# Optimization experiments

Hardware: AMD Instinct MI355X
Metric: run time of the kernel (lower is better)

Reference implementation:

```python
import jax, jax.numpy as jnp
import numpy as np
import math

B, S, D, H = 2, 2048, 1024, 16
DK = D // H


def setup_inputs() -> dict:
    key = jax.random.key(0)
    k1, k2, k3, k4, k5, k6 = jax.random.split(key, 6)
    scale = 1.0 / math.sqrt(D)
    return {
        "query": jax.random.normal(k1, (B, S, D), dtype=jnp.float32),
        "key": jax.random.normal(k2, (B, S, D), dtype=jnp.float32),
        "value": jax.random.normal(k3, (B, S, D), dtype=jnp.float32),
        "Wqkv": jax.random.normal(k4, (D, D), dtype=jnp.float32) * scale,
        "Wout": jax.random.normal(k5, (D, D), dtype=jnp.float32) * scale,
        "mask": jax.random.randint(k6, (B, 1, S, S), 0, 2, dtype=jnp.int32),
    }


def reference(query, key, value, Wqkv, Wout, mask):
    # Single shared QKV projection (same weight applied to q, k, v), no bias.
    q = query @ Wqkv.T
    k = key @ Wqkv.T
    v = value @ Wqkv.T
    # Faithful to the original: reshape (B, S, D) -> (B, H, S, DK) directly
    # (torch .reshape(n_batches, h, -1, d_k), NOT view+transpose).
    q = q.reshape(B, H, S, DK)
    k = k.reshape(B, H, S, DK)
    v = v.reshape(B, H, S, DK)
    scores = jnp.einsum("bhqd,bhkd->bhqk", q, k) / math.sqrt(DK)
    scores = jnp.where(mask == 0, jnp.float32(-1e9), scores)
    p_attn = jax.nn.softmax(scores, axis=-1)  # dropout is identity in eval
    x = jnp.einsum("bhqk,bhkd->bhqd", p_attn, v)  # [B,H,S,DK]
    x = x.transpose(0, 2, 1, 3).reshape(B, S, H * DK)
    return x @ Wout.T
```

## Files before the change

### kernel.cpp

```cpp
#include <hip/hip_runtime.h>
#include <stdint.h>


typedef __bf16 bf16;
typedef __bf16 bf16x8 __attribute__((ext_vector_type(8)));
typedef __bf16 bf16x4 __attribute__((ext_vector_type(4)));
typedef float f32x4 __attribute__((ext_vector_type(4)));

#define MFMA16(a, b, c) __builtin_amdgcn_mfma_f32_16x16x32_bf16((a), (b), (c), 0, 0, 0)
#define EXP2(x) __builtin_amdgcn_exp2f(x)

static constexpr int BATCH = 2;
static constexpr int SEQ = 2048;
static constexpr int DIM = 1024;
static constexpr int DK = 64;
static constexpr float QSCALE = 0.125f * 1.44269504088896340736f;

__device__ inline void gload16(const void* g, void* l) {
  __builtin_amdgcn_global_load_lds((const __attribute__((address_space(1))) void*)g,
                                   (__attribute__((address_space(3))) void*)l, 16, 0, 0);
}

__global__ __launch_bounds__(256) void mask_bits_kernel(const int* __restrict__ mask,
                                                        unsigned long long* __restrict__ bits) {
  int idx = blockIdx.x * 256 + threadIdx.x;
  int m = mask[idx];
  unsigned long long bal = __ballot(m != 0);
  if ((threadIdx.x & 63) == 0) bits[idx >> 6] = bal;
}

__global__ __launch_bounds__(256) void cvt_bf16_kernel(const float* __restrict__ s0,
                                                       const float* __restrict__ s1,
                                                       const float* __restrict__ s2,
                                                       const float* __restrict__ s3,
                                                       const float* __restrict__ s4,
                                                       bf16* __restrict__ d0, bf16* __restrict__ d1,
                                                       bf16* __restrict__ d2, bf16* __restrict__ d3,
                                                       bf16* __restrict__ d4) {
  const int y = blockIdx.y;
  const float* s = (y == 0) ? s0 : (y == 1) ? s1 : (y == 2) ? s2 : (y == 3) ? s3 : s4;
  bf16* d = (y == 0) ? d0 : (y == 1) ? d1 : (y == 2) ? d2 : (y == 3) ? d3 : d4;
  const int n8 = (y < 3) ? (BATCH * SEQ * DIM / 8) : (DIM * DIM / 8);
  for (int i = blockIdx.x * 256 + threadIdx.x; i < n8; i += gridDim.x * 256) {
    const float4 a = ((const float4*)s)[2 * i];
    const float4 b = ((const float4*)s)[2 * i + 1];
    bf16x8 v;
    v[0] = (bf16)a.x;
    v[1] = (bf16)a.y;
    v[2] = (bf16)a.z;
    v[3] = (bf16)a.w;
    v[4] = (bf16)b.x;
    v[5] = (bf16)b.y;
    v[6] = (bf16)b.z;
    v[7] = (bf16)b.w;
    ((bf16x8*)d)[i] = v;
  }
}

template <int BM, int NBY, int NBZ, typename TC>
__global__ __launch_bounds__(256) void gemm_bt_lds(const bf16* __restrict__ A0,
                                                   const bf16* __restrict__ A1,
                                                   const bf16* __restrict__ A2,
                                                   const bf16* __restrict__ W,
                                                   TC* __restrict__ C0,
                                                   TC* __restrict__ C1,
                                                   TC* __restrict__ C2,
                                                   float scale0) {
  constexpr int K = 1024, N = 1024;
  constexpr int MT = BM / 32;
  constexpr int NB = 8 * NBY * NBZ;
  __shared__ __align__(16) bf16 As[BM * 32];
  __shared__ __align__(16) bf16 Bs[128 * 32];

  const int lin = blockIdx.x + 8 * (blockIdx.y + NBY * blockIdx.z);
  const int l = (lin & 7) * (NB / 8) + (lin >> 3);
  const int lx = l & 7;
  const int lyz = l >> 3;
  const int ly = lyz % NBY;
  const int lz = lyz / NBY;

  const bf16* A = (lz == 0) ? A0 : (lz == 1) ? A1 : A2;
  TC* C = (lz == 0) ? C0 : (lz == 1) ? C1 : C2;
  const float sc = (lz == 0) ? scale0 : 1.0f;

  const int tid = threadIdx.x;
  const int lane = tid & 63;
  const int wv = tid >> 6;
  const int wm = wv >> 1, wn = wv & 1;
  const int lrow = lane & 15, quad = lane >> 4;
  const int m0 = ly * BM, n0 = lx * 128;

  const int r0 = tid >> 2, c0 = (tid & 3) * 8;
  const bf16* pa0 = A + (size_t)(m0 + r0) * K + c0;
  const bf16* pb0 = W + (size_t)(n0 + r0) * K + c0;
  const bf16* pb1 = W + (size_t)(n0 + 64 + r0) * K + c0;
  bf16* la0 = &As[tid * 8];
  bf16* lb0 = &Bs[tid * 8];
  bf16* lb1 = &Bs[2048 + tid * 8];
  const bf16* pa1 = nullptr;
  bf16* la1 = nullptr;
  if constexpr (BM == 128) {
    pa1 = A + (size_t)(m0 + 64 + r0) * K + c0;
    la1 = &As[2048 + tid * 8];
  }

  const f32x4 fz = {0.f, 0.f, 0.f, 0.f};
  f32x4 acc[MT][4];
#pragma unroll
  for (int i = 0; i < MT; ++i)
#pragma unroll
    for (int j = 0; j < 4; ++j) acc[i][j] = fz;

  for (int k0 = 0; k0 < K; k0 += 32) {
    __syncthreads();
    gload16(pa0 + k0, la0);
    if constexpr (BM == 128) gload16(pa1 + k0, la1);
    gload16(pb0 + k0, lb0);
    gload16(pb1 + k0, lb1);
    __syncthreads();
    bf16x8 af[MT], bfr[4];
#pragma unroll
    for (int mt = 0; mt < MT; ++mt)
      af[mt] = *(const bf16x8*)(&As[(wm * (BM / 2) + mt * 16 + lrow) * 32 + quad * 8]);
#pragma unroll
    for (int nt = 0; nt < 4; ++nt)
      bfr[nt] = *(const bf16x8*)(&Bs[(wn * 64 + nt * 16 + lrow) * 32 + quad * 8]);
#pragma unroll
    for (int mt = 0; mt < MT; ++mt)
#pragma unroll
      for (int nt = 0; nt < 4; ++nt) acc[mt][nt] = MFMA16(af[mt], bfr[nt], acc[mt][nt]);
  }

#pragma unroll
  for (int mt = 0; mt < MT; ++mt) {
    const int gm = m0 + wm * (BM / 2) + mt * 16 + quad * 4;
#pragma unroll
    for (int nt = 0; nt < 4; ++nt) {
      const int gn = n0 + wn * 64 + nt * 16 + lrow;
#pragma unroll
      for (int r = 0; r < 4; ++r) C[(size_t)(gm + r) * N + gn] = (TC)(acc[mt][nt][r] * sc);
    }
  }
}

__global__ __launch_bounds__(256, 2) void attn_kernel(const bf16* __restrict__ Qg,
                                                      const bf16* __restrict__ Kg,
                                                      const bf16* __restrict__ Vg,
                                                      const unsigned* __restrict__ bits,
                                                      bf16* __restrict__ Y) {
  constexpr int LQ = 72;
  __shared__ bf16 Qs[128 * LQ];
  __shared__ bf16 Ks[64 * LQ];
  __shared__ bf16 Vts[64 * LQ];
  __shared__ bf16 Ps[4][32 * LQ];

  const int tid = threadIdx.x;
  const int lane = tid & 63;
  const int wv = tid >> 6;
  const int lrow = lane & 15, quad = lane >> 4;
  const int bh = blockIdx.y;
  const int b = bh >> 4, h = bh & 15;
  const int q0 = blockIdx.x * 128;

  const bf16* Qh = Qg + (size_t)bh * (SEQ * DK);
  const bf16* Kh = Kg + (size_t)bh * (SEQ * DK);
  const bf16* Vh = Vg + (size_t)bh * (SEQ * DK);

#pragma unroll
  for (int i = 0; i < 4; ++i) {
    int s = tid + i * 256;
    int row = s >> 3, c8 = (s & 7) * 8;
    *(uint4*)(&Qs[row * LQ + c8]) = *(const uint4*)(Qh + (size_t)(q0 + row) * DK + c8);
  }

  const int krow = tid >> 3;
  const int kc8 = (tid & 7) * 8;
  const bf16* pk0 = Kh + (size_t)krow * DK + kc8;
  const bf16* pk1 = Kh + (size_t)(krow + 32) * DK + kc8;
  const int vn2 = tid & 31;
  const int vk2b = tid >> 5;
  const bf16* pv0 = Vh + (size_t)(vk2b + 0) * 2 * DK + vn2 * 2;
  const bf16* pv1 = Vh + (size_t)(vk2b + 8) * 2 * DK + vn2 * 2;
  const bf16* pv2 = Vh + (size_t)(vk2b + 16) * 2 * DK + vn2 * 2;
  const bf16* pv3 = Vh + (size_t)(vk2b + 24) * 2 * DK + vn2 * 2;

  uint4 kr0, kr1;
  uint32_t va[4], vb[4];

  kr0 = *(const uint4*)(pk0);
  kr1 = *(const uint4*)(pk1);
  va[0] = *(const uint32_t*)(pv0);
  vb[0] = *(const uint32_t*)(pv0 + DK);
  va[1] = *(const uint32_t*)(pv1);
  vb[1] = *(const uint32_t*)(pv1 + DK);
  va[2] = *(const uint32_t*)(pv2);
  vb[2] = *(const uint32_t*)(pv2 + DK);
  va[3] = *(const uint32_t*)(pv3);
  vb[3] = *(const uint32_t*)(pv3 + DK);
  *(uint4*)(&Ks[krow * LQ + kc8]) = kr0;
  *(uint4*)(&Ks[(krow + 32) * LQ + kc8]) = kr1;
#pragma unroll
  for (int i = 0; i < 4; ++i) {
    uint32_t t0 = (va[i] & 0xffffu) | (vb[i] << 16);
    uint32_t t1 = (va[i] >> 16) | (vb[i] & 0xffff0000u);
    *(uint32_t*)(&Vts[(vn2 * 2) * LQ + (vk2b + i * 8) * 2]) = t0;
    *(uint32_t*)(&Vts[(vn2 * 2 + 1) * LQ + (vk2b + i * 8) * 2]) = t1;
  }
  __syncthreads();

  bf16x8 qf[2][2];
#pragma unroll
  for (int nt = 0; nt < 2; ++nt)
#pragma unroll
    for (int ks = 0; ks < 2; ++ks)
      qf[nt][ks] = *(const bf16x8*)(&Qs[(wv * 32 + nt * 16 + lrow) * LQ + ks * 32 + quad * 8]);
  __syncthreads();

  const f32x4 fz = {0.f, 0.f, 0.f, 0.f};
  f32x4 of_t[4][2];
#pragma unroll
  for (int i = 0; i < 4; ++i)
#pragma unroll
    for (int j = 0; j < 2; ++j) of_t[i][j] = fz;
  float lsum[2] = {0.f, 0.f};

  const unsigned* bitrow = bits + (size_t)b * SEQ * (SEQ / 32);

  for (int kt = 0; kt < 32; ++kt) {
    const int cur = kt & 1;
    bf16* kb = cur ? Qs : Ks;
    bf16* vbuf = cur ? (Qs + 64 * LQ) : Vts;
    if (kt + 1 < 32) {
      const size_t adv = (size_t)(kt + 1) * 64 * DK;
      kr0 = *(const uint4*)(pk0 + adv);
      kr1 = *(const uint4*)(pk1 + adv);
      va[0] = *(const uint32_t*)(pv0 + adv);
      vb[0] = *(const uint32_t*)(pv0 + adv + DK);
      va[1] = *(const uint32_t*)(pv1 + adv);
      vb[1] = *(const uint32_t*)(pv1 + adv + DK);
      va[2] = *(const uint32_t*)(pv2 + adv);
      vb[2] = *(const uint32_t*)(pv2 + adv + DK);
      va[3] = *(const uint32_t*)(pv3 + adv);
      vb[3] = *(const uint32_t*)(pv3 + adv + DK);
    }
    uint2 mwn[2];
#pragma unroll
    for (int nt = 0; nt < 2; ++nt) {
      int row = q0 + wv * 32 + nt * 16 + lrow;
      mwn[nt] = *(const uint2*)(bitrow + (size_t)row * (SEQ / 32) + kt * 2);
    }

    f32x4 st[4][2];
#pragma unroll
    for (int mt = 0; mt < 4; ++mt)
#pragma unroll
      for (int nt = 0; nt < 2; ++nt) st[mt][nt] = fz;
#pragma unroll
    for (int ks = 0; ks < 2; ++ks) {
#pragma unroll
      for (int mt = 0; mt < 4; ++mt) {
        bf16x8 kfv = *(const bf16x8*)(kb + (mt * 16 + lrow) * LQ + ks * 32 + quad * 8);
#pragma unroll
        for (int nt = 0; nt < 2; ++nt) st[mt][nt] = MFMA16(kfv, qf[nt][ks], st[mt][nt]);
      }
    }

#pragma unroll
    for (int nt = 0; nt < 2; ++nt) {
      uint32_t ux = mwn[nt].x >> (quad * 4);
      uint32_t uy = mwn[nt].y >> (quad * 4);
      float psum = 0.f;
#pragma unroll
      for (int mt = 0; mt < 4; ++mt) {
        uint32_t u = (mt & 2) ? uy : ux;
        int sh = (mt & 1) << 4;
        bf16x4 pk;
#pragma unroll
        for (int r = 0; r < 4; ++r) {
          float p = EXP2(st[mt][nt][r]);
          p = ((u >> (sh + r)) & 1u) ? p : 0.f;
          psum += p;
          pk[r] = (bf16)p;
        }
        *(bf16x4*)(&Ps[wv][(nt * 16 + lrow) * LQ + mt * 16 + quad * 4]) = pk;
      }
      lsum[nt] += psum;
    }

#pragma unroll
    for (int ks = 0; ks < 2; ++ks) {
      bf16x8 avf[4], bpf[2];
#pragma unroll
      for (int dkt = 0; dkt < 4; ++dkt)
        avf[dkt] = *(const bf16x8*)(vbuf + (dkt * 16 + lrow) * LQ + ks * 32 + quad * 8);
#pragma unroll
      for (int rt = 0; rt < 2; ++rt)
        bpf[rt] = *(const bf16x8*)(&Ps[wv][(rt * 16 + lrow) * LQ + ks * 32 + quad * 8]);
#pragma unroll
      for (int dkt = 0; dkt < 4; ++dkt)
#pragma unroll
        for (int rt = 0; rt < 2; ++rt) of_t[dkt][rt] = MFMA16(avf[dkt], bpf[rt], of_t[dkt][rt]);
    }

    if (kt + 1 < 32) {
      bf16* kbn = cur ? Ks : Qs;
      bf16* vbn = cur ? Vts : (Qs + 64 * LQ);
      *(uint4*)(kbn + krow * LQ + kc8) = kr0;
      *(uint4*)(kbn + (krow + 32) * LQ + kc8) = kr1;
#pragma unroll
      for (int i = 0; i < 4; ++i) {
        uint32_t t0 = (va[i] & 0xffffu) | (vb[i] << 16);
        uint32_t t1 = (va[i] >> 16) | (vb[i] & 0xffff0000u);
        *(uint32_t*)(vbn + (vn2 * 2) * LQ + (vk2b + i * 8) * 2) = t0;
        *(uint32_t*)(vbn + (vn2 * 2 + 1) * LQ + (vk2b + i * 8) * 2) = t1;
      }
    }
    __syncthreads();
  }

  float linv[2];
#pragma unroll
  for (int nt = 0; nt < 2; ++nt) {
    float v = lsum[nt];
    v += __shfl_xor(v, 16);
    v += __shfl_xor(v, 32);
    linv[nt] = 1.0f / fmaxf(v, 1e-20f);
  }

#pragma unroll
  for (int dkt = 0; dkt < 4; ++dkt)
#pragma unroll
    for (int rt = 0; rt < 2; ++rt) {
      bf16x4 o;
#pragma unroll
      for (int j = 0; j < 4; ++j) o[j] = (bf16)(of_t[dkt][rt][j] * linv[rt]);
      const int row = q0 + wv * 32 + rt * 16 + lrow;
      *(bf16x4*)(&Y[((size_t)b * SEQ + row) * DIM + h * 64 + dkt * 16 + quad * 4]) = o;
    }
}

extern "C" void kernel_launch(void* const* d_in, const int* in_sizes, int n_in,
                              void* d_out, int out_size, void* d_ws, size_t ws_size,
                              hipStream_t stream) {
  const float* query = (const float*)d_in[0];
  const float* key = (const float*)d_in[1];
  const float* value = (const float*)d_in[2];
  const float* Wqkv = (const float*)d_in[3];
  const float* Wout = (const float*)d_in[4];
  const int* mask = (const int*)d_in[5];
  float* out = (float*)d_out;

  char* ws = (char*)d_ws;
  bf16* qin = (bf16*)(ws);
  bf16* kin = (bf16*)(ws + 8388608);
  bf16* vin = (bf16*)(ws + 16777216);
  bf16* Wq = (bf16*)(ws + 25165824);
  bf16* Wo = (bf16*)(ws + 27262976);
  bf16* q = (bf16*)(ws + 29360128);
  bf16* k = (bf16*)(ws + 37748736);
  bf16* v = (bf16*)(ws + 46137344);
  bf16* y = (bf16*)(ws);
  unsigned long long* bits64 = (unsigned long long*)(ws + 54525952);

  mask_bits_kernel<<<(BATCH * SEQ * SEQ) / 256, 256, 0, stream>>>(mask, bits64);

  cvt_bf16_kernel<<<dim3(256, 5), 256, 0, stream>>>(query, key, value, Wqkv, Wout,
                                                    qin, kin, vin, Wq, Wo);

  gemm_bt_lds<128, 32, 3, bf16>
      <<<dim3(8, 32, 3), 256, 0, stream>>>(qin, kin, vin, Wq, q, k, v, QSCALE);

  attn_kernel<<<dim3(16, 32), 256, 0, stream>>>(q, k, v, (const unsigned*)bits64, y);

  gemm_bt_lds<64, 64, 1, float>
      <<<dim3(8, 64, 1), 256, 0, stream>>>(y, y, y, Wo, out, out, out, 1.0f);
}
```

Before: 251.3 us.

## Double-buffer GEMM LDS tiles, prefetch mask bits, re-pad V transpose buffers

The projection GEMM now double-buffers its A and W LDS tiles. The next k-slice is issued via global_load_lds before the current slice's MFMAs run, and launch_bounds gains a min-blocks hint. In attention, the mask bit words are loaded one key tile ahead. V-transpose staging moves into two dedicated buffers with a 66-element row stride instead of reusing part of Qs. This aims to hide global latency and reduce LDS bank conflicts, but raises LDS use. The 132-byte row stride also leaves the 16-byte V fragment reads misaligned, which may split or slow those LDS loads.

```diff
diff --git a/kernel.cpp b/kernel.cpp
--- a/kernel.cpp
+++ b/kernel.cpp
@@ -58,19 +58,15 @@
 }
 
 template <int BM, int NBY, int NBZ, typename TC>
-__global__ __launch_bounds__(256) void gemm_bt_lds(const bf16* __restrict__ A0,
-                                                   const bf16* __restrict__ A1,
-                                                   const bf16* __restrict__ A2,
-                                                   const bf16* __restrict__ W,
-                                                   TC* __restrict__ C0,
-                                                   TC* __restrict__ C1,
-                                                   TC* __restrict__ C2,
-                                                   float scale0) {
+__global__ __launch_bounds__(256, (BM == 128) ? 3 : 2) void gemm_bt_lds(
+    const bf16* __restrict__ A0, const bf16* __restrict__ A1, const bf16* __restrict__ A2,
+    const bf16* __restrict__ W, TC* __restrict__ C0, TC* __restrict__ C1, TC* __restrict__ C2,
+    float scale0) {
   constexpr int K = 1024, N = 1024;
   constexpr int MT = BM / 32;
   constexpr int NB = 8 * NBY * NBZ;
-  __shared__ __align__(16) bf16 As[BM * 32];
-  __shared__ __align__(16) bf16 Bs[128 * 32];
+  __shared__ __align__(16) bf16 As[2][BM * 32];
+  __shared__ __align__(16) bf16 Bs[2][128 * 32];
 
   const int lin = blockIdx.x + 8 * (blockIdx.y + NBY * blockIdx.z);
   const int l = (lin & 7) * (NB / 8) + (lin >> 3);
@@ -94,15 +90,8 @@
   const bf16* pa0 = A + (size_t)(m0 + r0) * K + c0;
   const bf16* pb0 = W + (size_t)(n0 + r0) * K + c0;
   const bf16* pb1 = W + (size_t)(n0 + 64 + r0) * K + c0;
-  bf16* la0 = &As[tid * 8];
-  bf16* lb0 = &Bs[tid * 8];
-  bf16* lb1 = &Bs[2048 + tid * 8];
   const bf16* pa1 = nullptr;
-  bf16* la1 = nullptr;
-  if constexpr (BM == 128) {
-    pa1 = A + (size_t)(m0 + 64 + r0) * K + c0;
-    la1 = &As[2048 + tid * 8];
-  }
+  if constexpr (BM == 128) pa1 = A + (size_t)(m0 + 64 + r0) * K + c0;
 
   const f32x4 fz = {0.f, 0.f, 0.f, 0.f};
   f32x4 acc[MT][4];
@@ -111,24 +100,33 @@
 #pragma unroll
     for (int j = 0; j < 4; ++j) acc[i][j] = fz;
 
-  for (int k0 = 0; k0 < K; k0 += 32) {
+  gload16(pa0, &As[0][tid * 8]);
+  if constexpr (BM == 128) gload16(pa1, &As[0][2048 + tid * 8]);
+  gload16(pb0, &Bs[0][tid * 8]);
+  gload16(pb1, &Bs[0][2048 + tid * 8]);
+  __syncthreads();
+
+  for (int t = 0; t < K / 32; ++t) {
+    const int cur = t & 1;
+    if (t + 1 < K / 32) {
+      const int k1 = (t + 1) * 32;
+      gload16(pa0 + k1, &As[cur ^ 1][tid * 8]);
+      if constexpr (BM == 128) gload16(pa1 + k1, &As[cur ^ 1][2048 + tid * 8]);
+      gload16(pb0 + k1, &Bs[cur ^ 1][tid * 8]);
+      gload16(pb1 + k1, &Bs[cur ^ 1][2048 + tid * 8]);
+    }
+    bf16x8 af[MT], bfr[4];
+#pragma unroll
+    for (int mt = 0; mt < MT; ++mt)
+      af[mt] = *(const bf16x8*)(&As[cur][(wm * (BM / 2) + mt * 16 + lrow) * 32 + quad * 8]);
+#pragma unroll
+    for (int nt = 0; nt < 4; ++nt)
+      bfr[nt] = *(const bf16x8*)(&Bs[cur][(wn * 64 + nt * 16 + lrow) * 32 + quad * 8]);
+#pragma unroll
+    for (int mt = 0; mt < MT; ++mt)
+#pragma unroll
+      for (int nt = 0; nt < 4; ++nt) acc[mt][nt] = MFMA16(af[mt], bfr[nt], acc[mt][nt]);
     __syncthreads();
-    gload16(pa0 + k0, la0);
-    if constexpr (BM == 128) gload16(pa1 + k0, la1);
-    gload16(pb0 + k0, lb0);
-    gload16(pb1 + k0, lb1);
-    __syncthreads();
-    bf16x8 af[MT], bfr[4];
-#pragma unroll
-    for (int mt = 0; mt < MT; ++mt)
-      af[mt] = *(const bf16x8*)(&As[(wm * (BM / 2) + mt * 16 + lrow) * 32 + quad * 8]);
-#pragma unroll
-    for (int nt = 0; nt < 4; ++nt)
-      bfr[nt] = *(const bf16x8*)(&Bs[(wn * 64 + nt * 16 + lrow) * 32 + quad * 8]);
-#pragma unroll
-    for (int mt = 0; mt < MT; ++mt)
-#pragma unroll
-      for (int nt = 0; nt < 4; ++nt) acc[mt][nt] = MFMA16(af[mt], bfr[nt], acc[mt][nt]);
   }
 
 #pragma unroll
@@ -149,9 +147,11 @@
                                                       const unsigned* __restrict__ bits,
                                                       bf16* __restrict__ Y) {
   constexpr int LQ = 72;
+  constexpr int LV = 66;
   __shared__ bf16 Qs[128 * LQ];
   __shared__ bf16 Ks[64 * LQ];
-  __shared__ bf16 Vts[64 * LQ];
+  __shared__ bf16 Vt0[64 * LV];
+  __shared__ bf16 Vt1[64 * LV];
   __shared__ bf16 Ps[4][32 * LQ];
 
   const int tid = threadIdx.x;
@@ -203,8 +203,8 @@
   for (int i = 0; i < 4; ++i) {
     uint32_t t0 = (va[i] & 0xffffu) | (vb[i] << 16);
     uint32_t t1 = (va[i] >> 16) | (vb[i] & 0xffff0000u);
-    *(uint32_t*)(&Vts[(vn2 * 2) * LQ + (vk2b + i * 8) * 2]) = t0;
-    *(uint32_t*)(&Vts[(vn2 * 2 + 1) * LQ + (vk2b + i * 8) * 2]) = t1;
+    *(uint32_t*)(&Vt0[(vn2 * 2) * LV + (vk2b + i * 8) * 2]) = t0;
+    *(uint32_t*)(&Vt0[(vn2 * 2 + 1) * LV + (vk2b + i * 8) * 2]) = t1;
   }
   __syncthreads();
 
@@ -226,10 +226,18 @@
 
   const unsigned* bitrow = bits + (size_t)b * SEQ * (SEQ / 32);
 
+  uint2 mwn[2];
+#pragma unroll
+  for (int nt = 0; nt < 2; ++nt) {
+    int row = q0 + wv * 32 + nt * 16 + lrow;
+    mwn[nt] = *(const uint2*)(bitrow + (size_t)row * (SEQ / 32));
+  }
+
   for (int kt = 0; kt < 32; ++kt) {
     const int cur = kt & 1;
     bf16* kb = cur ? Qs : Ks;
-    bf16* vbuf = cur ? (Qs + 64 * LQ) : Vts;
+    bf16* vbuf = cur ? Vt1 : Vt0;
+    uint2 mwn_n[2];
     if (kt + 1 < 32) {
       const size_t adv = (size_t)(kt + 1) * 64 * DK;
       kr0 = *(const uint4*)(pk0 + adv);
@@ -242,12 +250,11 @@
       vb[2] = *(const uint32_t*)(pv2 + adv + DK);
       va[3] = *(const uint32_t*)(pv3 + adv);
       vb[3] = *(const uint32_t*)(pv3 + adv + DK);
-    }
-    uint2 mwn[2];
-#pragma unroll
-    for (int nt = 0; nt < 2; ++nt) {
-      int row = q0 + wv * 32 + nt * 16 + lrow;
-      mwn[nt] = *(const uint2*)(bitrow + (size_t)row * (SEQ / 32) + kt * 2);
+#pragma unroll
+      for (int nt = 0; nt < 2; ++nt) {
+        int row = q0 + wv * 32 + nt * 16 + lrow;
+        mwn_n[nt] = *(const uint2*)(bitrow + (size_t)row * (SEQ / 32) + (kt + 1) * 2);
+      }
     }
 
     f32x4 st[4][2];
@@ -292,7 +299,7 @@
       bf16x8 avf[4], bpf[2];
 #pragma unroll
       for (int dkt = 0; dkt < 4; ++dkt)
-        avf[dkt] = *(const bf16x8*)(vbuf + (dkt * 16 + lrow) * LQ + ks * 32 + quad * 8);
+        avf[dkt] = *(const bf16x8*)(vbuf + (dkt * 16 + lrow) * LV + ks * 32 + quad * 8);
 #pragma unroll
       for (int rt = 0; rt < 2; ++rt)
         bpf[rt] = *(const bf16x8*)(&Ps[wv][(rt * 16 + lrow) * LQ + ks * 32 + quad * 8]);
@@ -304,16 +311,18 @@
 
     if (kt + 1 < 32) {
       bf16* kbn = cur ? Ks : Qs;
-      bf16* vbn = cur ? Vts : (Qs + 64 * LQ);
+      bf16* vbn = cur ? Vt0 : Vt1;
       *(uint4*)(kbn + krow * LQ + kc8) = kr0;
       *(uint4*)(kbn + (krow + 32) * LQ + kc8) = kr1;
 #pragma unroll
       for (int i = 0; i < 4; ++i) {
         uint32_t t0 = (va[i] & 0xffffu) | (vb[i] << 16);
         uint32_t t1 = (va[i] >> 16) | (vb[i] & 0xffff0000u);
-        *(uint32_t*)(vbn + (vn2 * 2) * LQ + (vk2b + i * 8) * 2) = t0;
-        *(uint32_t*)(vbn + (vn2 * 2 + 1) * LQ + (vk2b + i * 8) * 2) = t1;
+        *(uint32_t*)(vbn + (vn2 * 2) * LV + (vk2b + i * 8) * 2) = t0;
+        *(uint32_t*)(vbn + (vn2 * 2 + 1) * LV + (vk2b + i * 8) * 2) = t1;
       }
+      mwn[0] = mwn_n[0];
+      mwn[1] = mwn_n[1];
     }
     __syncthreads();
   }
```

Result: slower. 286.5 us (+14.0%).
